# Kernel optimization log

Measured on AMD Instinct MI355X. Metric: run time of the kernel, lower is better.

The kernel has to match this reference:

```python
import jax, jax.numpy as jnp
import numpy as np

B, S = 4, 2048
IN_F, OUT_F = 4096, 4096
BLK = 8
NB_IN = IN_F // BLK   # 512
NB_OUT = OUT_F // BLK  # 512


def setup_inputs() -> dict:
    key = jax.random.key(0)
    k_x, k_c = jax.random.split(key)
    x = jax.random.normal(k_x, (B, S, IN_F), dtype=jnp.float32)
    # mimic xavier_uniform on (NB_OUT*NB_IN, BLK) then / sqrt(BLK)
    bound = float(np.sqrt(6.0 / (NB_OUT * NB_IN + BLK)))
    circ_params = jax.random.uniform(k_c, (NB_OUT, NB_IN, BLK), dtype=jnp.float32,
                                     minval=-bound, maxval=bound) / np.sqrt(BLK)
    bias = jnp.zeros((OUT_F,), dtype=jnp.float32)
    return {"x": x, "circ_params": circ_params, "bias": bias}


def reference(x, circ_params, bias):
    # x: (B, S, IN_F) -> (B, S, NB_IN, BLK)
    xb = x.reshape(*x.shape[:-1], NB_IN, BLK)
    x_rfft = jnp.fft.rfft(xb, axis=-1)              # (B, S, NB_IN, BLK//2+1) complex
    c_rfft = jnp.fft.rfft(circ_params, axis=-1)     # (NB_OUT, NB_IN, BLK//2+1) complex
    # per-frequency block contraction: sum over input blocks i
    out_rfft = jnp.einsum('bsif,nif->bsnf', x_rfft, c_rfft)  # (B, S, NB_OUT, BLK//2+1)
    out = jnp.fft.irfft(out_rfft, n=BLK, axis=-1)   # (B, S, NB_OUT, BLK)
    out = out.reshape(*x.shape[:-1], OUT_F)
    return out + bias
```

## Files before the change

kernel.cpp:

```cpp
#include <hip/hip_runtime.h>

#define AS1 __attribute__((address_space(1)))
#define AS3 __attribute__((address_space(3)))

typedef __attribute__((ext_vector_type(8))) short short8;
typedef __attribute__((ext_vector_type(4))) float floatx4;
typedef __attribute__((ext_vector_type(8))) unsigned short u16x8;
typedef __attribute__((ext_vector_type(4))) unsigned short u16x4;
typedef __attribute__((ext_vector_type(4))) float f32x4;

#define M_DIM 8192
#define K_DIM 4096
#define N_DIM 4096
#define NB    512

#define SQ2H 0.70710678118654752f

#define P0_OFF 0
#define P1_OFF 4194304
#define P2_OFF 12582912
#define P3_OFF 20971520
#define P4_OFF 29360128
#define Q0_OFF 0
#define Q1_OFF 262144
#define Q2_OFF 1310720
#define Q3_OFF 2359296
#define Q4_OFF 3407872

static __device__ __forceinline__ unsigned short f32_to_bf16(float f) {
  union { float f; unsigned int u; } v;
  v.f = f;
  return (unsigned short)((v.u + 0x7FFFu + ((v.u >> 16) & 1u)) >> 16);
}
static __device__ __forceinline__ float bf16_to_f32(unsigned short h) {
  union { unsigned int u; float f; } v;
  v.u = ((unsigned int)h) << 16;
  return v.f;
}

struct F8 { float a0, a4, r1, i1, r2, i2, r3, i3; };
static __device__ __forceinline__ F8 rfft8(const float* x) {
  F8 o;
  o.a0 = x[0]+x[1]+x[2]+x[3]+x[4]+x[5]+x[6]+x[7];
  o.a4 = x[0]-x[1]+x[2]-x[3]+x[4]-x[5]+x[6]-x[7];
  const float d1 = x[1]-x[3]-x[5]+x[7];
  const float s1 = x[1]+x[3]-x[5]-x[7];
  o.r1 = x[0]-x[4] + SQ2H*d1;
  o.i1 = -(SQ2H*s1 + x[2]-x[6]);
  o.r2 = x[0]-x[2]+x[4]-x[6];
  o.i2 = -(x[1]-x[3]+x[5]-x[7]);
  o.r3 = x[0]-x[4] - SQ2H*d1;
  o.i3 = -(SQ2H*s1 - x[2]+x[6]);
  return o;
}


__global__ __launch_bounds__(256) void xtransform_kernel(
    const float* __restrict__ x, unsigned short* __restrict__ XF)
{
  __shared__ alignas(16) float lds[8192];
  const int t  = threadIdx.x;
  const int m0 = blockIdx.x * 2;
  const float* src = x + (size_t)m0 * 4096;

#pragma unroll
  for (int s = 0; s < 8; ++s) {
    const int u  = s * 256 + t;
    const int pu = u ^ ((u >> 3) & 7);
    *reinterpret_cast<f32x4*>(lds + pu * 4) =
        *reinterpret_cast<const f32x4*>(src + (size_t)u * 4);
  }
  __syncthreads();

  const int r  = t >> 7;
  const int i4 = t & 127;
  float v[32];
#pragma unroll
  for (int p = 0; p < 8; ++p) {
    const int u  = r * 1024 + i4 * 8 + p;
    const int pu = u ^ ((u >> 3) & 7);
    *reinterpret_cast<f32x4*>(v + p * 4) = *reinterpret_cast<const f32x4*>(lds + pu * 4);
  }

  const int m = m0 + r;
  u16x4 p0, p4;
  u16x8 p1, p2, p3;
#pragma unroll
  for (int g = 0; g < 4; ++g) {
    F8 f = rfft8(v + g * 8);
    p0[g] = f32_to_bf16(f.a0);
    p4[g] = f32_to_bf16(f.a4);
    p1[2*g] = f32_to_bf16(f.r1); p1[2*g+1] = f32_to_bf16(f.i1);
    p2[2*g] = f32_to_bf16(f.r2); p2[2*g+1] = f32_to_bf16(f.i2);
    p3[2*g] = f32_to_bf16(f.r3); p3[2*g+1] = f32_to_bf16(f.i3);
  }
  *reinterpret_cast<u16x4*>(XF + P0_OFF + (size_t)m * 512 + i4 * 4) = p0;
  *reinterpret_cast<u16x4*>(XF + P4_OFF + (size_t)m * 512 + i4 * 4) = p4;
  *reinterpret_cast<u16x8*>(XF + P1_OFF + (size_t)m * 1024 + i4 * 8) = p1;
  *reinterpret_cast<u16x8*>(XF + P2_OFF + (size_t)m * 1024 + i4 * 8) = p2;
  *reinterpret_cast<u16x8*>(XF + P3_OFF + (size_t)m * 1024 + i4 * 8) = p3;
}

__global__ __launch_bounds__(256) void wtransform_kernel(
    const float* __restrict__ c, unsigned short* __restrict__ WF)
{
  const int tid = blockIdx.x * 256 + threadIdx.x;
  const int n = tid >> 9;
  const int i = tid & 511;
  float v[8];
  *reinterpret_cast<f32x4*>(v)     = *reinterpret_cast<const f32x4*>(c + (size_t)tid * 8);
  *reinterpret_cast<f32x4*>(v + 4) = *reinterpret_cast<const f32x4*>(c + (size_t)tid * 8 + 4);
  F8 f = rfft8(v);
  WF[Q0_OFF + (size_t)n * 512 + i] = f32_to_bf16(f.a0);
  WF[Q4_OFF + (size_t)n * 512 + i] = f32_to_bf16(f.a4);
  unsigned int q1or = (unsigned int)f32_to_bf16(f.r1) | ((unsigned int)f32_to_bf16(-f.i1) << 16);
  unsigned int q1oi = (unsigned int)f32_to_bf16(f.i1) | ((unsigned int)f32_to_bf16(f.r1) << 16);
  unsigned int q2or = (unsigned int)f32_to_bf16(f.r2) | ((unsigned int)f32_to_bf16(-f.i2) << 16);
  unsigned int q2oi = (unsigned int)f32_to_bf16(f.i2) | ((unsigned int)f32_to_bf16(f.r2) << 16);
  unsigned int q3or = (unsigned int)f32_to_bf16(f.r3) | ((unsigned int)f32_to_bf16(-f.i3) << 16);
  unsigned int q3oi = (unsigned int)f32_to_bf16(f.i3) | ((unsigned int)f32_to_bf16(f.r3) << 16);
  *reinterpret_cast<unsigned int*>(WF + Q1_OFF + (size_t)n * 1024 + 2 * i)         = q1or;
  *reinterpret_cast<unsigned int*>(WF + Q1_OFF + (size_t)(512 + n) * 1024 + 2 * i) = q1oi;
  *reinterpret_cast<unsigned int*>(WF + Q2_OFF + (size_t)n * 1024 + 2 * i)         = q2or;
  *reinterpret_cast<unsigned int*>(WF + Q2_OFF + (size_t)(512 + n) * 1024 + 2 * i) = q2oi;
  *reinterpret_cast<unsigned int*>(WF + Q3_OFF + (size_t)n * 1024 + 2 * i)         = q3or;
  *reinterpret_cast<unsigned int*>(WF + Q3_OFF + (size_t)(512 + n) * 1024 + 2 * i) = q3oi;
}

__global__ __launch_bounds__(256) void gemm_freq_kernel(
    const unsigned short* __restrict__ XF,
    const unsigned short* __restrict__ WF,
    unsigned short* __restrict__ OF)
{
  const int bid = blockIdx.x;
  const int swz = (bid & 7) * 256 + (bid >> 3);
  const int mt  = swz >> 5;
  const int yf  = swz & 31;
  int z, nt;
  if (yf < 4)       { z = 0; nt = yf; }
  else if (yf < 28) { z = 1 + ((yf - 4) >> 3); nt = (yf - 4) & 7; }
  else              { z = 4; nt = yf - 28; }

  int K, aoff, boff;
  switch (z) {
    case 0:  K = 512;  aoff = P0_OFF; boff = Q0_OFF; break;
    case 1:  K = 1024; aoff = P1_OFF; boff = Q1_OFF; break;
    case 2:  K = 1024; aoff = P2_OFF; boff = Q2_OFF; break;
    case 3:  K = 1024; aoff = P3_OFF; boff = Q3_OFF; break;
    default: K = 512;  aoff = P4_OFF; boff = Q4_OFF; break;
  }
  const int n0 = nt * 128;
  const int m0 = mt * 128;

  const unsigned short* A  = XF + aoff;
  const unsigned short* Bm = WF + boff;
  unsigned short* C        = OF + aoff;

  __shared__ alignas(16) unsigned short As[128 * 64];
  __shared__ alignas(16) unsigned short Bs[128 * 64];

  const int tid  = threadIdx.x;
  const int lane = tid & 63;
  const int wave = tid >> 6;
  const int wm   = wave >> 1;
  const int wn   = wave & 1;
  const int quad = lane >> 4;
  const int l15  = lane & 15;
  const int par4 = (l15 & 1) << 2;

  floatx4 acc[4][4];
#pragma unroll
  for (int i = 0; i < 4; ++i)
#pragma unroll
    for (int j = 0; j < 4; ++j) acc[i][j] = (floatx4){0.f, 0.f, 0.f, 0.f};

  for (int k0 = 0; k0 < K; k0 += 64) {
#pragma unroll
    for (int j = 0; j < 4; ++j) {
      const int c   = j * 256 + wave * 64 + lane;
      const int row = c >> 3;
      const int lu  = (c & 7) ^ ((row & 1) << 2);
      const unsigned short* ga = A  + (size_t)(m0 + row) * K + k0 + lu * 8;
      const unsigned short* gb = Bm + (size_t)(n0 + row) * K + k0 + lu * 8;
      __builtin_amdgcn_global_load_lds((AS1 void*)ga, (AS3 void*)(As + c * 8), 16, 0, 0);
      __builtin_amdgcn_global_load_lds((AS1 void*)gb, (AS3 void*)(Bs + c * 8), 16, 0, 0);
    }
    __syncthreads();

#pragma unroll
    for (int s = 0; s < 2; ++s) {
      const int u = (s * 4 + quad) ^ par4;
      short8 af[4], bf[4];
#pragma unroll
      for (int mi = 0; mi < 4; ++mi)
        af[mi] = *reinterpret_cast<const short8*>(As + (wm * 64 + mi * 16 + l15) * 64 + u * 8);
#pragma unroll
      for (int ni = 0; ni < 4; ++ni)
        bf[ni] = *reinterpret_cast<const short8*>(Bs + (wn * 64 + ni * 16 + l15) * 64 + u * 8);
#pragma unroll
      for (int mi = 0; mi < 4; ++mi)
#pragma unroll
        for (int ni = 0; ni < 4; ++ni)
          acc[mi][ni] = __builtin_amdgcn_mfma_f32_16x16x32_bf16(
              af[mi], bf[ni], acc[mi][ni], 0, 0, 0);
    }
    __syncthreads();
  }

#pragma unroll
  for (int mi = 0; mi < 4; ++mi) {
#pragma unroll
    for (int r = 0; r < 4; ++r) {
      const int grow = m0 + wm * 64 + mi * 16 + quad * 4 + r;
      unsigned short* crow = C + (size_t)grow * K;
#pragma unroll
      for (int ni = 0; ni < 4; ++ni)
        crow[n0 + wn * 64 + ni * 16 + l15] = f32_to_bf16(acc[mi][ni][r]);
    }
  }
}

__global__ __launch_bounds__(256) void irfft_kernel(
    const unsigned short* __restrict__ OF,
    const float* __restrict__ bias,
    float* __restrict__ out)
{
  __shared__ alignas(16) float lds[256 * 36];
  const int t   = threadIdx.x;
  const int gt  = blockIdx.x * 256 + t;
  const int m   = gt >> 7;
  const int nb4 = gt & 127;

  const u16x4 a0v = *reinterpret_cast<const u16x4*>(OF + P0_OFF + (size_t)m * 512 + nb4 * 4);
  const u16x4 a4v = *reinterpret_cast<const u16x4*>(OF + P4_OFF + (size_t)m * 512 + nb4 * 4);
  const u16x4 r1v = *reinterpret_cast<const u16x4*>(OF + P1_OFF + (size_t)m * 1024 + nb4 * 4);
  const u16x4 i1v = *reinterpret_cast<const u16x4*>(OF + P1_OFF + (size_t)m * 1024 + 512 + nb4 * 4);
  const u16x4 r2v = *reinterpret_cast<const u16x4*>(OF + P2_OFF + (size_t)m * 1024 + nb4 * 4);
  const u16x4 i2v = *reinterpret_cast<const u16x4*>(OF + P2_OFF + (size_t)m * 1024 + 512 + nb4 * 4);
  const u16x4 r3v = *reinterpret_cast<const u16x4*>(OF + P3_OFF + (size_t)m * 1024 + nb4 * 4);
  const u16x4 i3v = *reinterpret_cast<const u16x4*>(OF + P3_OFF + (size_t)m * 1024 + 512 + nb4 * 4);

  float res[32];
#pragma unroll
  for (int j = 0; j < 4; ++j) {
    const int nblk = nb4 * 4 + j;
    const float a0 = bf16_to_f32(a0v[j]), a4 = bf16_to_f32(a4v[j]);
    const float r1 = bf16_to_f32(r1v[j]), i1 = bf16_to_f32(i1v[j]);
    const float r2 = bf16_to_f32(r2v[j]), i2 = bf16_to_f32(i2v[j]);
    const float r3 = bf16_to_f32(r3v[j]), i3 = bf16_to_f32(i3v[j]);

    const float ep = a0 + a4, em = a0 - a4;
    const float sr1 = SQ2H * r1, si1 = SQ2H * i1;
    const float sr3 = SQ2H * r3, si3 = SQ2H * i3;
    float o[8];
    o[0] = (ep + 2.f * ( r1 + r2 + r3)) * 0.125f;
    o[1] = (em + 2.f * ( sr1 - si1 - i2 - sr3 - si3)) * 0.125f;
    o[2] = (ep + 2.f * (-i1 - r2 + i3)) * 0.125f;
    o[3] = (em + 2.f * (-sr1 - si1 + i2 + sr3 - si3)) * 0.125f;
    o[4] = (ep + 2.f * (-r1 + r2 - r3)) * 0.125f;
    o[5] = (em + 2.f * (-sr1 + si1 - i2 + sr3 + si3)) * 0.125f;
    o[6] = (ep + 2.f * ( i1 - r2 - i3)) * 0.125f;
    o[7] = (em + 2.f * ( sr1 + si1 + i2 - sr3 + si3)) * 0.125f;

    const f32x4 blo = *reinterpret_cast<const f32x4*>(bias + nblk * 8);
    const f32x4 bhi = *reinterpret_cast<const f32x4*>(bias + nblk * 8 + 4);
#pragma unroll
    for (int k = 0; k < 4; ++k) {
      res[j * 8 + k]     = o[k]     + blo[k];
      res[j * 8 + 4 + k] = o[k + 4] + bhi[k];
    }
  }

  float* dst = lds + t * 36;
#pragma unroll
  for (int p = 0; p < 8; ++p)
    *reinterpret_cast<f32x4*>(dst + p * 4) = *reinterpret_cast<const f32x4*>(res + p * 4);
  __syncthreads();

  float* gbase = out + (size_t)blockIdx.x * 8192;
#pragma unroll
  for (int s = 0; s < 8; ++s) {
    const int off16 = s * 256 + t;
    const f32x4 vv = *reinterpret_cast<const f32x4*>(
        lds + (off16 >> 3) * 36 + (off16 & 7) * 4);
    *reinterpret_cast<f32x4*>(gbase + off16 * 4) = vv;
  }
}


__global__ __launch_bounds__(256) void convert_x_kernel(
    const float* __restrict__ x, unsigned short* __restrict__ Xb)
{
  const size_t t = (size_t)blockIdx.x * 256 + threadIdx.x;
  const f32x4 a = *reinterpret_cast<const f32x4*>(x + t * 8);
  const f32x4 b = *reinterpret_cast<const f32x4*>(x + t * 8 + 4);
  union { u16x8 v; unsigned short s[8]; } o;
#pragma unroll
  for (int u = 0; u < 4; ++u) { o.s[u] = f32_to_bf16(a[u]); o.s[u + 4] = f32_to_bf16(b[u]); }
  *reinterpret_cast<u16x8*>(Xb + t * 8) = o.v;
}

__global__ __launch_bounds__(256) void expand_w_kernel(
    const float* __restrict__ c, unsigned short* __restrict__ W)
{
  const int tid = blockIdx.x * 256 + threadIdx.x;
  const int o = tid >> 9, i = tid & 511, n = o >> 3, t = o & 7;
  const float* src = c + ((size_t)(n * NB + i) << 3);
  float raw[8];
  *reinterpret_cast<f32x4*>(raw)     = *reinterpret_cast<const f32x4*>(src);
  *reinterpret_cast<f32x4*>(raw + 4) = *reinterpret_cast<const f32x4*>(src + 4);
  union { u16x8 v; unsigned short s[8]; } outv;
#pragma unroll
  for (int u = 0; u < 8; ++u) outv.s[u] = f32_to_bf16(raw[(t - u) & 7]);
  *reinterpret_cast<u16x8*>(W + (size_t)o * K_DIM + i * 8) = outv.v;
}

__global__ __launch_bounds__(256) void gemm_bt_kernel(
    const unsigned short* __restrict__ A, const unsigned short* __restrict__ Bm,
    const float* __restrict__ bias, float* __restrict__ C)
{
  __shared__ alignas(16) unsigned short As[128 * 32];
  __shared__ alignas(16) unsigned short Bs[128 * 32];
  const int tid = threadIdx.x, lane = tid & 63, wave = tid >> 6;
  const int wm = wave >> 1, wn = wave & 1;
  const int m0 = blockIdx.y * 128, n0 = blockIdx.x * 128;
  const int quad = lane >> 4, l15 = lane & 15;

  floatx4 acc[4][4];
#pragma unroll
  for (int i = 0; i < 4; ++i)
#pragma unroll
    for (int j = 0; j < 4; ++j) acc[i][j] = (floatx4){0.f, 0.f, 0.f, 0.f};

  for (int k0 = 0; k0 < K_DIM; k0 += 32) {
#pragma unroll
    for (int j = 0; j < 2; ++j) {
      const int chunk = j * 256 + wave * 64 + lane;
      const int row = chunk >> 2, kc = (chunk & 3) << 3;
      const unsigned short* ga = A  + (size_t)(m0 + row) * K_DIM + (k0 + kc);
      const unsigned short* gb = Bm + (size_t)(n0 + row) * K_DIM + (k0 + kc);
      unsigned short* la = As + (j * 256 + wave * 64) * 8;
      unsigned short* lb = Bs + (j * 256 + wave * 64) * 8;
      __builtin_amdgcn_global_load_lds((AS1 void*)ga, (AS3 void*)la, 16, 0, 0);
      __builtin_amdgcn_global_load_lds((AS1 void*)gb, (AS3 void*)lb, 16, 0, 0);
    }
    __syncthreads();
    short8 af[4], bf[4];
#pragma unroll
    for (int mi = 0; mi < 4; ++mi)
      af[mi] = *reinterpret_cast<const short8*>(As + (wm * 64 + mi * 16 + l15) * 32 + quad * 8);
#pragma unroll
    for (int ni = 0; ni < 4; ++ni)
      bf[ni] = *reinterpret_cast<const short8*>(Bs + (wn * 64 + ni * 16 + l15) * 32 + quad * 8);
#pragma unroll
    for (int mi = 0; mi < 4; ++mi)
#pragma unroll
      for (int ni = 0; ni < 4; ++ni)
        acc[mi][ni] = __builtin_amdgcn_mfma_f32_16x16x32_bf16(af[mi], bf[ni], acc[mi][ni], 0, 0, 0);
    __syncthreads();
  }
  float bv[4]; int cols[4];
#pragma unroll
  for (int ni = 0; ni < 4; ++ni) { cols[ni] = n0 + wn * 64 + ni * 16 + l15; bv[ni] = bias[cols[ni]]; }
#pragma unroll
  for (int mi = 0; mi < 4; ++mi)
#pragma unroll
    for (int r = 0; r < 4; ++r) {
      const int grow = m0 + wm * 64 + mi * 16 + quad * 4 + r;
      float* crow = C + (size_t)grow * N_DIM;
#pragma unroll
      for (int ni = 0; ni < 4; ++ni) crow[cols[ni]] = acc[mi][ni][r] + bv[ni];
    }
}

extern "C" void kernel_launch(void* const* d_in, const int* in_sizes, int n_in,
                              void* d_out, int out_size, void* d_ws, size_t ws_size,
                              hipStream_t stream) {
  const float* x    = (const float*)d_in[0];
  const float* circ = (const float*)d_in[1];
  const float* bias = (const float*)d_in[2];
  float* out = (float*)d_out;

  const size_t XF_BYTES = (size_t)33554432 * 2;
  const size_t WF_BYTES = (size_t)3670016 * 2;
  const size_t OF_BYTES = (size_t)33554432 * 2;
  const size_t NEED = XF_BYTES + WF_BYTES + OF_BYTES;

  if (ws_size >= NEED) {
    unsigned short* XF = (unsigned short*)d_ws;
    unsigned short* WF = (unsigned short*)((char*)d_ws + XF_BYTES);
    unsigned short* OF = (unsigned short*)((char*)d_ws + XF_BYTES + WF_BYTES);

    wtransform_kernel<<<(NB * NB) / 256, 256, 0, stream>>>(circ, WF);
    xtransform_kernel<<<M_DIM / 2, 256, 0, stream>>>(x, XF);
    gemm_freq_kernel<<<2048, 256, 0, stream>>>(XF, WF, OF);
    irfft_kernel<<<M_DIM / 2, 256, 0, stream>>>(OF, bias, out);
  } else {
    unsigned short* W  = (unsigned short*)d_ws;
    unsigned short* Xb = (unsigned short*)((char*)d_ws + (size_t)N_DIM * K_DIM * 2);
    convert_x_kernel<<<(M_DIM * K_DIM / 8) / 256, 256, 0, stream>>>(x, Xb);
    expand_w_kernel<<<(N_DIM * NB) / 256, 256, 0, stream>>>(circ, W);
    dim3 grid(N_DIM / 128, M_DIM / 128);
    gemm_bt_kernel<<<grid, 256, 0, stream>>>(Xb, W, bias, out);
  }
}
```

Before: 348.4 us.

## Fuse frequency GEMMs with inverse FFT epilogue and merge prep kernels

```diff
diff --git a/kernel.cpp b/kernel.cpp
--- a/kernel.cpp
+++ b/kernel.cpp
@@ -31,11 +31,6 @@
   union { float f; unsigned int u; } v;
   v.f = f;
   return (unsigned short)((v.u + 0x7FFFu + ((v.u >> 16) & 1u)) >> 16);
-}
-static __device__ __forceinline__ float bf16_to_f32(unsigned short h) {
-  union { unsigned int u; float f; } v;
-  v.u = ((unsigned int)h) << 16;
-  return v.f;
 }
 
 struct F8 { float a0, a4, r1, i1, r2, i2, r3, i3; };
@@ -55,12 +50,40 @@
 }
 
 
-__global__ __launch_bounds__(256) void xtransform_kernel(
-    const float* __restrict__ x, unsigned short* __restrict__ XF)
+__global__ __launch_bounds__(256) void prep_kernel(
+    const float* __restrict__ x, const float* __restrict__ circ,
+    unsigned short* __restrict__ XF, unsigned short* __restrict__ WF)
 {
   __shared__ alignas(16) float lds[8192];
-  const int t  = threadIdx.x;
-  const int m0 = blockIdx.x * 2;
+  const int t = threadIdx.x;
+
+  if (blockIdx.x < 1024) {
+    const int tid = blockIdx.x * 256 + t;
+    const int n = tid >> 9;
+    const int i = tid & 511;
+    float v[8];
+    *reinterpret_cast<f32x4*>(v)     = *reinterpret_cast<const f32x4*>(circ + (size_t)tid * 8);
+    *reinterpret_cast<f32x4*>(v + 4) = *reinterpret_cast<const f32x4*>(circ + (size_t)tid * 8 + 4);
+    F8 f = rfft8(v);
+    WF[Q0_OFF + (size_t)n * 512 + i] = f32_to_bf16(f.a0);
+    WF[Q4_OFF + (size_t)n * 512 + i] = f32_to_bf16(f.a4);
+    unsigned int q1or = (unsigned int)f32_to_bf16(f.r1) | ((unsigned int)f32_to_bf16(-f.i1) << 16);
+    unsigned int q1oi = (unsigned int)f32_to_bf16(f.i1) | ((unsigned int)f32_to_bf16(f.r1) << 16);
+    unsigned int q2or = (unsigned int)f32_to_bf16(f.r2) | ((unsigned int)f32_to_bf16(-f.i2) << 16);
+    unsigned int q2oi = (unsigned int)f32_to_bf16(f.i2) | ((unsigned int)f32_to_bf16(f.r2) << 16);
+    unsigned int q3or = (unsigned int)f32_to_bf16(f.r3) | ((unsigned int)f32_to_bf16(-f.i3) << 16);
+    unsigned int q3oi = (unsigned int)f32_to_bf16(f.i3) | ((unsigned int)f32_to_bf16(f.r3) << 16);
+    *reinterpret_cast<unsigned int*>(WF + Q1_OFF + (size_t)n * 1024 + 2 * i)         = q1or;
+    *reinterpret_cast<unsigned int*>(WF + Q1_OFF + (size_t)(512 + n) * 1024 + 2 * i) = q1oi;
+    *reinterpret_cast<unsigned int*>(WF + Q2_OFF + (size_t)n * 1024 + 2 * i)         = q2or;
+    *reinterpret_cast<unsigned int*>(WF + Q2_OFF + (size_t)(512 + n) * 1024 + 2 * i) = q2oi;
+    *reinterpret_cast<unsigned int*>(WF + Q3_OFF + (size_t)n * 1024 + 2 * i)         = q3or;
+    *reinterpret_cast<unsigned int*>(WF + Q3_OFF + (size_t)(512 + n) * 1024 + 2 * i) = q3oi;
+    return;
+  }
+
+  const int bx = blockIdx.x - 1024;
+  const int m0 = bx * 2;
   const float* src = x + (size_t)m0 * 4096;
 
 #pragma unroll
@@ -101,63 +124,67 @@
   *reinterpret_cast<u16x8*>(XF + P3_OFF + (size_t)m * 1024 + i4 * 8) = p3;
 }
 
-__global__ __launch_bounds__(256) void wtransform_kernel(
-    const float* __restrict__ c, unsigned short* __restrict__ WF)
-{
-  const int tid = blockIdx.x * 256 + threadIdx.x;
-  const int n = tid >> 9;
-  const int i = tid & 511;
-  float v[8];
-  *reinterpret_cast<f32x4*>(v)     = *reinterpret_cast<const f32x4*>(c + (size_t)tid * 8);
-  *reinterpret_cast<f32x4*>(v + 4) = *reinterpret_cast<const f32x4*>(c + (size_t)tid * 8 + 4);
-  F8 f = rfft8(v);
-  WF[Q0_OFF + (size_t)n * 512 + i] = f32_to_bf16(f.a0);
-  WF[Q4_OFF + (size_t)n * 512 + i] = f32_to_bf16(f.a4);
-  unsigned int q1or = (unsigned int)f32_to_bf16(f.r1) | ((unsigned int)f32_to_bf16(-f.i1) << 16);
-  unsigned int q1oi = (unsigned int)f32_to_bf16(f.i1) | ((unsigned int)f32_to_bf16(f.r1) << 16);
-  unsigned int q2or = (unsigned int)f32_to_bf16(f.r2) | ((unsigned int)f32_to_bf16(-f.i2) << 16);
-  unsigned int q2oi = (unsigned int)f32_to_bf16(f.i2) | ((unsigned int)f32_to_bf16(f.r2) << 16);
-  unsigned int q3or = (unsigned int)f32_to_bf16(f.r3) | ((unsigned int)f32_to_bf16(-f.i3) << 16);
-  unsigned int q3oi = (unsigned int)f32_to_bf16(f.i3) | ((unsigned int)f32_to_bf16(f.r3) << 16);
-  *reinterpret_cast<unsigned int*>(WF + Q1_OFF + (size_t)n * 1024 + 2 * i)         = q1or;
-  *reinterpret_cast<unsigned int*>(WF + Q1_OFF + (size_t)(512 + n) * 1024 + 2 * i) = q1oi;
-  *reinterpret_cast<unsigned int*>(WF + Q2_OFF + (size_t)n * 1024 + 2 * i)         = q2or;
-  *reinterpret_cast<unsigned int*>(WF + Q2_OFF + (size_t)(512 + n) * 1024 + 2 * i) = q2oi;
-  *reinterpret_cast<unsigned int*>(WF + Q3_OFF + (size_t)n * 1024 + 2 * i)         = q3or;
-  *reinterpret_cast<unsigned int*>(WF + Q3_OFF + (size_t)(512 + n) * 1024 + 2 * i) = q3oi;
-}
-
-__global__ __launch_bounds__(256) void gemm_freq_kernel(
+#define PLANE_LOOP(KZ, APL, QPL, ACC_R, ACC_I, CPLX)                          \
+  for (int k0 = 0; k0 < (KZ); k0 += 64) {                                     \
+    _Pragma("unroll")                                                         \
+    for (int j_ = 0; j_ < 4; ++j_) {                                          \
+      const int c_   = j_ * 256 + tid;                                        \
+      const int row_ = c_ >> 3;                                               \
+      const int lu_  = (c_ & 7) ^ ((row_ & 1) << 2);                          \
+      const unsigned short* ga_ = (APL) + (size_t)(m0 + row_) * (KZ) + k0 + lu_ * 8; \
+      __builtin_amdgcn_global_load_lds((AS1 void*)ga_, (AS3 void*)(As + c_ * 8), 16, 0, 0); \
+    }                                                                         \
+    {                                                                         \
+      const int r0_  = tid >> 3;                                              \
+      const int lu0_ = (tid & 7) ^ ((r0_ & 1) << 2);                          \
+      const unsigned short* gb0_ = (QPL) + (size_t)(n0b + r0_) * (KZ) + k0 + lu0_ * 8; \
+      __builtin_amdgcn_global_load_lds((AS1 void*)gb0_, (AS3 void*)(Bs + tid * 8), 16, 0, 0); \
+      if (CPLX) {                                                             \
+        const int c1_  = 256 + tid;                                           \
+        const int rl_  = c1_ >> 3;                                \
+        const int lu1_ = (c1_ & 7) ^ ((rl_ & 1) << 2);                        \
+        const unsigned short* gb1_ = (QPL) + (size_t)(512 + n0b + (rl_ - 32)) * (KZ) + k0 + lu1_ * 8; \
+        __builtin_amdgcn_global_load_lds((AS1 void*)gb1_, (AS3 void*)(Bs + c1_ * 8), 16, 0, 0); \
+      }                                                                       \
+    }                                                                         \
+    __syncthreads();                                                          \
+    _Pragma("unroll")                                                         \
+    for (int s_ = 0; s_ < 2; ++s_) {                                          \
+      const int u_ = (s_ * 4 + quad) ^ par4;                                  \
+      short8 af_[4];                                                          \
+      _Pragma("unroll")                                                       \
+      for (int mi_ = 0; mi_ < 4; ++mi_)                                       \
+        af_[mi_] = *reinterpret_cast<const short8*>(As + (wm * 64 + mi_ * 16 + l15) * 64 + u_ * 8); \
+      const short8 br_ = *reinterpret_cast<const short8*>(Bs + (wn * 16 + l15) * 64 + u_ * 8); \
+      _Pragma("unroll")                                                       \
+      for (int mi_ = 0; mi_ < 4; ++mi_)                                       \
+        ACC_R[mi_] = __builtin_amdgcn_mfma_f32_16x16x32_bf16(af_[mi_], br_, ACC_R[mi_], 0, 0, 0); \
+      if (CPLX) {                                                             \
+        const short8 bi_ = *reinterpret_cast<const short8*>(Bs + (32 + wn * 16 + l15) * 64 + u_ * 8); \
+        _Pragma("unroll")                                                     \
+        for (int mi_ = 0; mi_ < 4; ++mi_)                                     \
+          ACC_I[mi_] = __builtin_amdgcn_mfma_f32_16x16x32_bf16(af_[mi_], bi_, ACC_I[mi_], 0, 0, 0); \
+      }                                                                       \
+    }                                                                         \
+    __syncthreads();                                                          \
+  }
+
+__global__ __launch_bounds__(256) void gemm_fused_kernel(
     const unsigned short* __restrict__ XF,
     const unsigned short* __restrict__ WF,
-    unsigned short* __restrict__ OF)
+    const float* __restrict__ bias,
+    float* __restrict__ out)
 {
   const int bid = blockIdx.x;
-  const int swz = (bid & 7) * 256 + (bid >> 3);
-  const int mt  = swz >> 5;
-  const int yf  = swz & 31;
-  int z, nt;
-  if (yf < 4)       { z = 0; nt = yf; }
-  else if (yf < 28) { z = 1 + ((yf - 4) >> 3); nt = (yf - 4) & 7; }
-  else              { z = 4; nt = yf - 28; }
-
-  int K, aoff, boff;
-  switch (z) {
-    case 0:  K = 512;  aoff = P0_OFF; boff = Q0_OFF; break;
-    case 1:  K = 1024; aoff = P1_OFF; boff = Q1_OFF; break;
-    case 2:  K = 1024; aoff = P2_OFF; boff = Q2_OFF; break;
-    case 3:  K = 1024; aoff = P3_OFF; boff = Q3_OFF; break;
-    default: K = 512;  aoff = P4_OFF; boff = Q4_OFF; break;
-  }
-  const int n0 = nt * 128;
-  const int m0 = mt * 128;
-
-  const unsigned short* A  = XF + aoff;
-  const unsigned short* Bm = WF + boff;
-  unsigned short* C        = OF + aoff;
+  const int xcd = bid & 7;
+  const int idx = bid >> 3;
+  const int mt  = (xcd >> 1) * 16 + (idx >> 3);
+  const int nt  = (xcd & 1) * 8 + (idx & 7);
+  const int m0  = mt * 128;
+  const int n0b = nt * 32;
 
   __shared__ alignas(16) unsigned short As[128 * 64];
-  __shared__ alignas(16) unsigned short Bs[128 * 64];
+  __shared__ alignas(16) unsigned short Bs[64 * 64];
 
   const int tid  = threadIdx.x;
   const int lane = tid & 63;
@@ -168,122 +195,55 @@
   const int l15  = lane & 15;
   const int par4 = (l15 & 1) << 2;
 
-  floatx4 acc[4][4];
-#pragma unroll
-  for (int i = 0; i < 4; ++i)
-#pragma unroll
-    for (int j = 0; j < 4; ++j) acc[i][j] = (floatx4){0.f, 0.f, 0.f, 0.f};
-
-  for (int k0 = 0; k0 < K; k0 += 64) {
-#pragma unroll
-    for (int j = 0; j < 4; ++j) {
-      const int c   = j * 256 + wave * 64 + lane;
-      const int row = c >> 3;
-      const int lu  = (c & 7) ^ ((row & 1) << 2);
-      const unsigned short* ga = A  + (size_t)(m0 + row) * K + k0 + lu * 8;
-      const unsigned short* gb = Bm + (size_t)(n0 + row) * K + k0 + lu * 8;
-      __builtin_amdgcn_global_load_lds((AS1 void*)ga, (AS3 void*)(As + c * 8), 16, 0, 0);
-      __builtin_amdgcn_global_load_lds((AS1 void*)gb, (AS3 void*)(Bs + c * 8), 16, 0, 0);
+  floatx4 a0c[4], a4c[4], c1r[4], c1i[4], c2r[4], c2i[4], c3r[4], c3i[4];
+#pragma unroll
+  for (int i = 0; i < 4; ++i) {
+    a0c[i] = (floatx4){0.f,0.f,0.f,0.f}; a4c[i] = (floatx4){0.f,0.f,0.f,0.f};
+    c1r[i] = (floatx4){0.f,0.f,0.f,0.f}; c1i[i] = (floatx4){0.f,0.f,0.f,0.f};
+    c2r[i] = (floatx4){0.f,0.f,0.f,0.f}; c2i[i] = (floatx4){0.f,0.f,0.f,0.f};
+    c3r[i] = (floatx4){0.f,0.f,0.f,0.f}; c3i[i] = (floatx4){0.f,0.f,0.f,0.f};
+  }
+
+  PLANE_LOOP(512,  XF + P0_OFF, WF + Q0_OFF, a0c, a0c, 0)
+  PLANE_LOOP(1024, XF + P1_OFF, WF + Q1_OFF, c1r, c1i, 1)
+  PLANE_LOOP(1024, XF + P2_OFF, WF + Q2_OFF, c2r, c2i, 1)
+  PLANE_LOOP(1024, XF + P3_OFF, WF + Q3_OFF, c3r, c3i, 1)
+  PLANE_LOOP(512,  XF + P4_OFF, WF + Q4_OFF, a4c, a4c, 0)
+
+  const int colb = n0b + wn * 16 + l15;
+  const f32x4 blo = *reinterpret_cast<const f32x4*>(bias + colb * 8);
+  const f32x4 bhi = *reinterpret_cast<const f32x4*>(bias + colb * 8 + 4);
+
+#pragma unroll
+  for (int mi = 0; mi < 4; ++mi) {
+#pragma unroll
+    for (int rg = 0; rg < 4; ++rg) {
+      const float a0 = a0c[mi][rg], a4 = a4c[mi][rg];
+      const float r1 = c1r[mi][rg], i1 = c1i[mi][rg];
+      const float r2 = c2r[mi][rg], i2 = c2i[mi][rg];
+      const float r3 = c3r[mi][rg], i3 = c3i[mi][rg];
+
+      const float ep = a0 + a4, em = a0 - a4;
+      const float sr1 = SQ2H * r1, si1 = SQ2H * i1;
+      const float sr3 = SQ2H * r3, si3 = SQ2H * i3;
+      float o[8];
+      o[0] = (ep + 2.f * ( r1 + r2 + r3)) * 0.125f;
+      o[1] = (em + 2.f * ( sr1 - si1 - i2 - sr3 - si3)) * 0.125f;
+      o[2] = (ep + 2.f * (-i1 - r2 + i3)) * 0.125f;
+      o[3] = (em + 2.f * (-sr1 - si1 + i2 + sr3 - si3)) * 0.125f;
+      o[4] = (ep + 2.f * (-r1 + r2 - r3)) * 0.125f;
+      o[5] = (em + 2.f * (-sr1 + si1 - i2 + sr3 + si3)) * 0.125f;
+      o[6] = (ep + 2.f * ( i1 - r2 - i3)) * 0.125f;
+      o[7] = (em + 2.f * ( sr1 + si1 + i2 - sr3 + si3)) * 0.125f;
+
+      f32x4 lo, hi;
+#pragma unroll
+      for (int tt = 0; tt < 4; ++tt) { lo[tt] = o[tt] + blo[tt]; hi[tt] = o[tt + 4] + bhi[tt]; }
+      const int mrow = m0 + wm * 64 + mi * 16 + quad * 4 + rg;
+      float* dst = out + (size_t)mrow * N_DIM + colb * 8;
+      *reinterpret_cast<f32x4*>(dst)     = lo;
+      *reinterpret_cast<f32x4*>(dst + 4) = hi;
     }
-    __syncthreads();
-
-#pragma unroll
-    for (int s = 0; s < 2; ++s) {
-      const int u = (s * 4 + quad) ^ par4;
-      short8 af[4], bf[4];
-#pragma unroll
-      for (int mi = 0; mi < 4; ++mi)
-        af[mi] = *reinterpret_cast<const short8*>(As + (wm * 64 + mi * 16 + l15) * 64 + u * 8);
-#pragma unroll
-      for (int ni = 0; ni < 4; ++ni)
-        bf[ni] = *reinterpret_cast<const short8*>(Bs + (wn * 64 + ni * 16 + l15) * 64 + u * 8);
-#pragma unroll
-      for (int mi = 0; mi < 4; ++mi)
-#pragma unroll
-        for (int ni = 0; ni < 4; ++ni)
-          acc[mi][ni] = __builtin_amdgcn_mfma_f32_16x16x32_bf16(
-              af[mi], bf[ni], acc[mi][ni], 0, 0, 0);
-    }
-    __syncthreads();
-  }
-
-#pragma unroll
-  for (int mi = 0; mi < 4; ++mi) {
-#pragma unroll
-    for (int r = 0; r < 4; ++r) {
-      const int grow = m0 + wm * 64 + mi * 16 + quad * 4 + r;
-      unsigned short* crow = C + (size_t)grow * K;
-#pragma unroll
-      for (int ni = 0; ni < 4; ++ni)
-        crow[n0 + wn * 64 + ni * 16 + l15] = f32_to_bf16(acc[mi][ni][r]);
-    }
-  }
-}
-
-__global__ __launch_bounds__(256) void irfft_kernel(
-    const unsigned short* __restrict__ OF,
-    const float* __restrict__ bias,
-    float* __restrict__ out)
-{
-  __shared__ alignas(16) float lds[256 * 36];
-  const int t   = threadIdx.x;
-  const int gt  = blockIdx.x * 256 + t;
-  const int m   = gt >> 7;
-  const int nb4 = gt & 127;
-
-  const u16x4 a0v = *reinterpret_cast<const u16x4*>(OF + P0_OFF + (size_t)m * 512 + nb4 * 4);
-  const u16x4 a4v = *reinterpret_cast<const u16x4*>(OF + P4_OFF + (size_t)m * 512 + nb4 * 4);
-  const u16x4 r1v = *reinterpret_cast<const u16x4*>(OF + P1_OFF + (size_t)m * 1024 + nb4 * 4);
-  const u16x4 i1v = *reinterpret_cast<const u16x4*>(OF + P1_OFF + (size_t)m * 1024 + 512 + nb4 * 4);
-  const u16x4 r2v = *reinterpret_cast<const u16x4*>(OF + P2_OFF + (size_t)m * 1024 + nb4 * 4);
-  const u16x4 i2v = *reinterpret_cast<const u16x4*>(OF + P2_OFF + (size_t)m * 1024 + 512 + nb4 * 4);
-  const u16x4 r3v = *reinterpret_cast<const u16x4*>(OF + P3_OFF + (size_t)m * 1024 + nb4 * 4);
-  const u16x4 i3v = *reinterpret_cast<const u16x4*>(OF + P3_OFF + (size_t)m * 1024 + 512 + nb4 * 4);
-
-  float res[32];
-#pragma unroll
-  for (int j = 0; j < 4; ++j) {
-    const int nblk = nb4 * 4 + j;
-    const float a0 = bf16_to_f32(a0v[j]), a4 = bf16_to_f32(a4v[j]);
-    const float r1 = bf16_to_f32(r1v[j]), i1 = bf16_to_f32(i1v[j]);
-    const float r2 = bf16_to_f32(r2v[j]), i2 = bf16_to_f32(i2v[j]);
-    const float r3 = bf16_to_f32(r3v[j]), i3 = bf16_to_f32(i3v[j]);
-
-    const float ep = a0 + a4, em = a0 - a4;
-    const float sr1 = SQ2H * r1, si1 = SQ2H * i1;
-    const float sr3 = SQ2H * r3, si3 = SQ2H * i3;
-    float o[8];
-    o[0] = (ep + 2.f * ( r1 + r2 + r3)) * 0.125f;
-    o[1] = (em + 2.f * ( sr1 - si1 - i2 - sr3 - si3)) * 0.125f;
-    o[2] = (ep + 2.f * (-i1 - r2 + i3)) * 0.125f;
-    o[3] = (em + 2.f * (-sr1 - si1 + i2 + sr3 - si3)) * 0.125f;
-    o[4] = (ep + 2.f * (-r1 + r2 - r3)) * 0.125f;
-    o[5] = (em + 2.f * (-sr1 + si1 - i2 + sr3 + si3)) * 0.125f;
-    o[6] = (ep + 2.f * ( i1 - r2 - i3)) * 0.125f;
-    o[7] = (em + 2.f * ( sr1 + si1 + i2 - sr3 + si3)) * 0.125f;
-
-    const f32x4 blo = *reinterpret_cast<const f32x4*>(bias + nblk * 8);
-    const f32x4 bhi = *reinterpret_cast<const f32x4*>(bias + nblk * 8 + 4);
-#pragma unroll
-    for (int k = 0; k < 4; ++k) {
-      res[j * 8 + k]     = o[k]     + blo[k];
-      res[j * 8 + 4 + k] = o[k + 4] + bhi[k];
-    }
-  }
-
-  float* dst = lds + t * 36;
-#pragma unroll
-  for (int p = 0; p < 8; ++p)
-    *reinterpret_cast<f32x4*>(dst + p * 4) = *reinterpret_cast<const f32x4*>(res + p * 4);
-  __syncthreads();
-
-  float* gbase = out + (size_t)blockIdx.x * 8192;
-#pragma unroll
-  for (int s = 0; s < 8; ++s) {
-    const int off16 = s * 256 + t;
-    const f32x4 vv = *reinterpret_cast<const f32x4*>(
-        lds + (off16 >> 3) * 36 + (off16 & 7) * 4);
-    *reinterpret_cast<f32x4*>(gbase + off16 * 4) = vv;
   }
 }
 
@@ -383,18 +343,14 @@
 
   const size_t XF_BYTES = (size_t)33554432 * 2;
   const size_t WF_BYTES = (size_t)3670016 * 2;
-  const size_t OF_BYTES = (size_t)33554432 * 2;
-  const size_t NEED = XF_BYTES + WF_BYTES + OF_BYTES;
+  const size_t NEED = XF_BYTES + WF_BYTES;
 
   if (ws_size >= NEED) {
     unsigned short* XF = (unsigned short*)d_ws;
     unsigned short* WF = (unsigned short*)((char*)d_ws + XF_BYTES);
-    unsigned short* OF = (unsigned short*)((char*)d_ws + XF_BYTES + WF_BYTES);
-
-    wtransform_kernel<<<(NB * NB) / 256, 256, 0, stream>>>(circ, WF);
-    xtransform_kernel<<<M_DIM / 2, 256, 0, stream>>>(x, XF);
-    gemm_freq_kernel<<<2048, 256, 0, stream>>>(XF, WF, OF);
-    irfft_kernel<<<M_DIM / 2, 256, 0, stream>>>(OF, bias, out);
+
+    prep_kernel<<<1024 + M_DIM / 2, 256, 0, stream>>>(x, circ, XF, WF);
+    gemm_fused_kernel<<<1024, 256, 0, stream>>>(XF, WF, bias, out);
   } else {
     unsigned short* W  = (unsigned short*)d_ws;
     unsigned short* Xb = (unsigned short*)((char*)d_ws + (size_t)N_DIM * K_DIM * 2);
```

Result: slower. 472.2 us (+35.5%).

## Merge W/X transforms into one launch and double-buffer GEMM LDS tiles

Applied to the files above, without the earlier changes.

```diff
diff --git a/kernel.cpp b/kernel.cpp
--- a/kernel.cpp
+++ b/kernel.cpp
@@ -55,12 +55,40 @@
 }
 
 
-__global__ __launch_bounds__(256) void xtransform_kernel(
-    const float* __restrict__ x, unsigned short* __restrict__ XF)
+__global__ __launch_bounds__(256) void prep_kernel(
+    const float* __restrict__ x, const float* __restrict__ circ,
+    unsigned short* __restrict__ XF, unsigned short* __restrict__ WF)
 {
   __shared__ alignas(16) float lds[8192];
-  const int t  = threadIdx.x;
-  const int m0 = blockIdx.x * 2;
+  const int t = threadIdx.x;
+
+  if (blockIdx.x < 1024) {
+    const int tid = blockIdx.x * 256 + t;
+    const int n = tid >> 9;
+    const int i = tid & 511;
+    float v[8];
+    *reinterpret_cast<f32x4*>(v)     = *reinterpret_cast<const f32x4*>(circ + (size_t)tid * 8);
+    *reinterpret_cast<f32x4*>(v + 4) = *reinterpret_cast<const f32x4*>(circ + (size_t)tid * 8 + 4);
+    F8 f = rfft8(v);
+    WF[Q0_OFF + (size_t)n * 512 + i] = f32_to_bf16(f.a0);
+    WF[Q4_OFF + (size_t)n * 512 + i] = f32_to_bf16(f.a4);
+    unsigned int q1or = (unsigned int)f32_to_bf16(f.r1) | ((unsigned int)f32_to_bf16(-f.i1) << 16);
+    unsigned int q1oi = (unsigned int)f32_to_bf16(f.i1) | ((unsigned int)f32_to_bf16(f.r1) << 16);
+    unsigned int q2or = (unsigned int)f32_to_bf16(f.r2) | ((unsigned int)f32_to_bf16(-f.i2) << 16);
+    unsigned int q2oi = (unsigned int)f32_to_bf16(f.i2) | ((unsigned int)f32_to_bf16(f.r2) << 16);
+    unsigned int q3or = (unsigned int)f32_to_bf16(f.r3) | ((unsigned int)f32_to_bf16(-f.i3) << 16);
+    unsigned int q3oi = (unsigned int)f32_to_bf16(f.i3) | ((unsigned int)f32_to_bf16(f.r3) << 16);
+    *reinterpret_cast<unsigned int*>(WF + Q1_OFF + (size_t)n * 1024 + 2 * i)         = q1or;
+    *reinterpret_cast<unsigned int*>(WF + Q1_OFF + (size_t)(512 + n) * 1024 + 2 * i) = q1oi;
+    *reinterpret_cast<unsigned int*>(WF + Q2_OFF + (size_t)n * 1024 + 2 * i)         = q2or;
+    *reinterpret_cast<unsigned int*>(WF + Q2_OFF + (size_t)(512 + n) * 1024 + 2 * i) = q2oi;
+    *reinterpret_cast<unsigned int*>(WF + Q3_OFF + (size_t)n * 1024 + 2 * i)         = q3or;
+    *reinterpret_cast<unsigned int*>(WF + Q3_OFF + (size_t)(512 + n) * 1024 + 2 * i) = q3oi;
+    return;
+  }
+
+  const int bx = blockIdx.x - 1024;
+  const int m0 = bx * 2;
   const float* src = x + (size_t)m0 * 4096;
 
 #pragma unroll
@@ -101,31 +129,36 @@
   *reinterpret_cast<u16x8*>(XF + P3_OFF + (size_t)m * 1024 + i4 * 8) = p3;
 }
 
-__global__ __launch_bounds__(256) void wtransform_kernel(
-    const float* __restrict__ c, unsigned short* __restrict__ WF)
-{
-  const int tid = blockIdx.x * 256 + threadIdx.x;
-  const int n = tid >> 9;
-  const int i = tid & 511;
-  float v[8];
-  *reinterpret_cast<f32x4*>(v)     = *reinterpret_cast<const f32x4*>(c + (size_t)tid * 8);
-  *reinterpret_cast<f32x4*>(v + 4) = *reinterpret_cast<const f32x4*>(c + (size_t)tid * 8 + 4);
-  F8 f = rfft8(v);
-  WF[Q0_OFF + (size_t)n * 512 + i] = f32_to_bf16(f.a0);
-  WF[Q4_OFF + (size_t)n * 512 + i] = f32_to_bf16(f.a4);
-  unsigned int q1or = (unsigned int)f32_to_bf16(f.r1) | ((unsigned int)f32_to_bf16(-f.i1) << 16);
-  unsigned int q1oi = (unsigned int)f32_to_bf16(f.i1) | ((unsigned int)f32_to_bf16(f.r1) << 16);
-  unsigned int q2or = (unsigned int)f32_to_bf16(f.r2) | ((unsigned int)f32_to_bf16(-f.i2) << 16);
-  unsigned int q2oi = (unsigned int)f32_to_bf16(f.i2) | ((unsigned int)f32_to_bf16(f.r2) << 16);
-  unsigned int q3or = (unsigned int)f32_to_bf16(f.r3) | ((unsigned int)f32_to_bf16(-f.i3) << 16);
-  unsigned int q3oi = (unsigned int)f32_to_bf16(f.i3) | ((unsigned int)f32_to_bf16(f.r3) << 16);
-  *reinterpret_cast<unsigned int*>(WF + Q1_OFF + (size_t)n * 1024 + 2 * i)         = q1or;
-  *reinterpret_cast<unsigned int*>(WF + Q1_OFF + (size_t)(512 + n) * 1024 + 2 * i) = q1oi;
-  *reinterpret_cast<unsigned int*>(WF + Q2_OFF + (size_t)n * 1024 + 2 * i)         = q2or;
-  *reinterpret_cast<unsigned int*>(WF + Q2_OFF + (size_t)(512 + n) * 1024 + 2 * i) = q2oi;
-  *reinterpret_cast<unsigned int*>(WF + Q3_OFF + (size_t)n * 1024 + 2 * i)         = q3or;
-  *reinterpret_cast<unsigned int*>(WF + Q3_OFF + (size_t)(512 + n) * 1024 + 2 * i) = q3oi;
-}
+#define STAGE(AsB, BsB, step)                                                 \
+  {                                                                           \
+    const int kk_ = (step) * 32;                                              \
+    _Pragma("unroll")                                                         \
+    for (int j_ = 0; j_ < 2; ++j_) {                                          \
+      const int c_   = j_ * 256 + tid;                            \
+      const int row_ = c_ >> 2;                                   \
+      const int lu_  = (c_ & 3) ^ ((row_ >> 1) & 3);                          \
+      const unsigned short* ga_ = A  + (size_t)(m0 + row_) * K + kk_ + lu_ * 8; \
+      const unsigned short* gb_ = Bm + (size_t)(n0 + row_) * K + kk_ + lu_ * 8; \
+      __builtin_amdgcn_global_load_lds((AS1 void*)ga_, (AS3 void*)((AsB) + c_ * 8), 16, 0, 0); \
+      __builtin_amdgcn_global_load_lds((AS1 void*)gb_, (AS3 void*)((BsB) + c_ * 8), 16, 0, 0); \
+    }                                                                         \
+  }
+
+#define COMPUTE(AsB, BsB)                                                     \
+  {                                                                           \
+    short8 af_[4], bf_[4];                                                    \
+    _Pragma("unroll")                                                         \
+    for (int mi_ = 0; mi_ < 4; ++mi_)                                         \
+      af_[mi_] = *reinterpret_cast<const short8*>((AsB) + (wm * 64 + mi_ * 16 + l15) * 32 + ua * 8); \
+    _Pragma("unroll")                                                         \
+    for (int ni_ = 0; ni_ < 4; ++ni_)                                         \
+      bf_[ni_] = *reinterpret_cast<const short8*>((BsB) + (wn * 64 + ni_ * 16 + l15) * 32 + ua * 8); \
+    _Pragma("unroll")                                                         \
+    for (int mi_ = 0; mi_ < 4; ++mi_)                                         \
+      _Pragma("unroll")                                                       \
+      for (int ni_ = 0; ni_ < 4; ++ni_)                                       \
+        acc[mi_][ni_] = __builtin_amdgcn_mfma_f32_16x16x32_bf16(af_[mi_], bf_[ni_], acc[mi_][ni_], 0, 0, 0); \
+  }
 
 __global__ __launch_bounds__(256) void gemm_freq_kernel(
     const unsigned short* __restrict__ XF,
@@ -156,8 +189,10 @@
   const unsigned short* Bm = WF + boff;
   unsigned short* C        = OF + aoff;
 
-  __shared__ alignas(16) unsigned short As[128 * 64];
-  __shared__ alignas(16) unsigned short Bs[128 * 64];
+  __shared__ alignas(16) unsigned short As0[128 * 32];
+  __shared__ alignas(16) unsigned short Bs0[128 * 32];
+  __shared__ alignas(16) unsigned short As1[128 * 32];
+  __shared__ alignas(16) unsigned short Bs1[128 * 32];
 
   const int tid  = threadIdx.x;
   const int lane = tid & 63;
@@ -166,7 +201,7 @@
   const int wn   = wave & 1;
   const int quad = lane >> 4;
   const int l15  = lane & 15;
-  const int par4 = (l15 & 1) << 2;
+  const int ua   = quad ^ ((l15 >> 1) & 3);
 
   floatx4 acc[4][4];
 #pragma unroll
@@ -174,36 +209,16 @@
 #pragma unroll
     for (int j = 0; j < 4; ++j) acc[i][j] = (floatx4){0.f, 0.f, 0.f, 0.f};
 
-  for (int k0 = 0; k0 < K; k0 += 64) {
-#pragma unroll
-    for (int j = 0; j < 4; ++j) {
-      const int c   = j * 256 + wave * 64 + lane;
-      const int row = c >> 3;
-      const int lu  = (c & 7) ^ ((row & 1) << 2);
-      const unsigned short* ga = A  + (size_t)(m0 + row) * K + k0 + lu * 8;
-      const unsigned short* gb = Bm + (size_t)(n0 + row) * K + k0 + lu * 8;
-      __builtin_amdgcn_global_load_lds((AS1 void*)ga, (AS3 void*)(As + c * 8), 16, 0, 0);
-      __builtin_amdgcn_global_load_lds((AS1 void*)gb, (AS3 void*)(Bs + c * 8), 16, 0, 0);
-    }
+  STAGE(As0, Bs0, 0);
+  __syncthreads();
+
+  const int nsteps = K >> 5;
+  for (int t = 0; t < nsteps; t += 2) {
+    STAGE(As1, Bs1, t + 1);
+    COMPUTE(As0, Bs0);
     __syncthreads();
-
-#pragma unroll
-    for (int s = 0; s < 2; ++s) {
-      const int u = (s * 4 + quad) ^ par4;
-      short8 af[4], bf[4];
-#pragma unroll
-      for (int mi = 0; mi < 4; ++mi)
-        af[mi] = *reinterpret_cast<const short8*>(As + (wm * 64 + mi * 16 + l15) * 64 + u * 8);
-#pragma unroll
-      for (int ni = 0; ni < 4; ++ni)
-        bf[ni] = *reinterpret_cast<const short8*>(Bs + (wn * 64 + ni * 16 + l15) * 64 + u * 8);
-#pragma unroll
-      for (int mi = 0; mi < 4; ++mi)
-#pragma unroll
-        for (int ni = 0; ni < 4; ++ni)
-          acc[mi][ni] = __builtin_amdgcn_mfma_f32_16x16x32_bf16(
-              af[mi], bf[ni], acc[mi][ni], 0, 0, 0);
-    }
+    if (t + 2 < nsteps) STAGE(As0, Bs0, t + 2);
+    COMPUTE(As1, Bs1);
     __syncthreads();
   }
 
@@ -391,8 +406,7 @@
     unsigned short* WF = (unsigned short*)((char*)d_ws + XF_BYTES);
     unsigned short* OF = (unsigned short*)((char*)d_ws + XF_BYTES + WF_BYTES);
 
-    wtransform_kernel<<<(NB * NB) / 256, 256, 0, stream>>>(circ, WF);
-    xtransform_kernel<<<M_DIM / 2, 256, 0, stream>>>(x, XF);
+    prep_kernel<<<1024 + M_DIM / 2, 256, 0, stream>>>(x, circ, XF, WF);
     gemm_freq_kernel<<<2048, 256, 0, stream>>>(XF, WF, OF);
     irfft_kernel<<<M_DIM / 2, 256, 0, stream>>>(OF, bias, out);
   } else {
```

Measured after the change: 348.2 us. Within noise of the previous version (-0.1%).
